# Performance work log

Measured on AMD Instinct MI355X. Metric: run time of the kernel, lower is better.

The kernel has to match this reference:

```python
import jax, jax.numpy as jnp
import numpy as np

B = 64
H = 768  # hidden_dim; x is [B, H, H], split along dim 1 into Q, D of [B, H//2, H]


def setup_inputs() -> dict:
    key = jax.random.key(0)
    kx, kw, kb = jax.random.split(key, 3)
    x = jax.random.normal(kx, (B, H, H), dtype=jnp.float32)
    # nn.Linear(H, H): weight [out, in], bias [out]
    W = jax.random.normal(kw, (H, H), dtype=jnp.float32) * (1.0 / np.sqrt(H))
    b = jax.random.normal(kb, (H,), dtype=jnp.float32) * 0.01
    return {"x": x, "W": W, "b": b}


def reference(x, W, b):
    T = H // 2
    Q = x[:, :T, :]          # [B, T, H]
    D = x[:, T:2 * T, :]     # [B, T, H]
    # Q = tanh(Linear(Q)); torch Linear: y = x @ W^T + b
    Q = jnp.tanh(jnp.einsum('bth,oh->bto', Q, W) + b)  # [B, T, H]
    D_t = jnp.swapaxes(D, 1, 2)                         # [B, H, T]
    L = jnp.einsum('bth,bsh->bts', Q, D)                # [B, T, T]
    A_Q = jnp.swapaxes(jax.nn.softmax(L, axis=1), 1, 2) # softmax over dim 1, then transpose -> [B, T, T]
    C_Q = jnp.matmul(D_t, A_Q)                          # [B, H, T]
    Q_t = jnp.swapaxes(Q, 1, 2)                         # [B, H, T]
    A_D = jax.nn.softmax(L, axis=2)                     # [B, T, T]
    C_D = jnp.matmul(jnp.concatenate((Q_t, C_Q), axis=1), A_D)  # [B, 2H, T]
    C_D_t = jnp.swapaxes(C_D, 1, 2)                     # [B, T, 2H]
    return jnp.concatenate((C_D_t, D), axis=2)          # [B, T, 3H]
```

## Files before the change

kernel.cpp:

```cpp
#include <hip/hip_runtime.h>


typedef __bf16 bf16x8 __attribute__((ext_vector_type(8)));
typedef __bf16 bf16x4 __attribute__((ext_vector_type(4)));
typedef float  f32x4  __attribute__((ext_vector_type(4)));

#define HH 768
#define TT 384

__device__ inline void split8(const float* __restrict__ p, bf16x8& hi, bf16x8& lo) {
    float4 f0 = *(const float4*)p;
    float4 f1 = *(const float4*)(p + 4);
    float f[8] = {f0.x, f0.y, f0.z, f0.w, f1.x, f1.y, f1.z, f1.w};
#pragma unroll
    for (int i = 0; i < 8; i++) {
        __bf16 h = (__bf16)f[i];
        hi[i] = h;
        lo[i] = (__bf16)(f[i] - (float)h);
    }
}

__device__ inline void split8r(float4 f0, float4 f1, bf16x8& hi, bf16x8& lo) {
    float f[8] = {f0.x, f0.y, f0.z, f0.w, f1.x, f1.y, f1.z, f1.w};
#pragma unroll
    for (int i = 0; i < 8; i++) {
        __bf16 h = (__bf16)f[i];
        hi[i] = h;
        lo[i] = (__bf16)(f[i] - (float)h);
    }
}

__device__ inline void gload16(const void* g, void* l) {
    __builtin_amdgcn_global_load_lds(
        (const __attribute__((address_space(1))) unsigned int*)g,
        (__attribute__((address_space(3))) unsigned int*)l, 16, 0, 0);
}

__global__ void splitW_kernel(const float* __restrict__ W, __bf16* __restrict__ Whi,
                              __bf16* __restrict__ Wlo) {
    int idx = blockIdx.x * 256 + threadIdx.x;
    bf16x8 h, l;
    split8(W + (size_t)idx * 8, h, l);
    *(bf16x8*)&Whi[(size_t)idx * 8] = h;
    *(bf16x8*)&Wlo[(size_t)idx * 8] = l;
}

__global__ __launch_bounds__(256) void fused_g1prep_kernel(
    const float* __restrict__ x, const __bf16* __restrict__ Whi,
    const __bf16* __restrict__ Wlo, const float* __restrict__ bias,
    __bf16* __restrict__ Qhi, __bf16* __restrict__ Qlo, __bf16* __restrict__ M4,
    __bf16* __restrict__ Dt, float* __restrict__ out) {
    __shared__ __align__(16) char smem[49152];
    const int tid = threadIdx.x;
    if (blockIdx.x >= 1152) {
        float (*tile)[33] = (float(*)[33])smem;
        int pid = blockIdx.x - 1152;
        int hb = pid % 24, sb = (pid / 24) % 12, b = pid / 288;
        int h0 = hb * 32, s0 = sb * 32;
        int tx = tid & 31, ty = tid >> 5;
        const float* src = x + ((size_t)b * HH + TT) * HH;
        float* outb = out + (size_t)b * TT * 2304;
#pragma unroll
        for (int j = 0; j < 4; j++) {
            int s = s0 + ty + 8 * j, h = h0 + tx;
            float v = src[(size_t)s * HH + h];
            tile[ty + 8 * j][tx] = v;
            outb[(size_t)s * 2304 + 1536 + h] = v;
        }
        __syncthreads();
        __bf16* Dtb = Dt + (size_t)b * HH * TT;
#pragma unroll
        for (int j = 0; j < 4; j++) {
            int h = h0 + ty + 8 * j, s = s0 + tx;
            Dtb[(size_t)h * TT + s] = (__bf16)tile[tx][ty + 8 * j];
        }
        return;
    }
    __bf16* Ah = (__bf16*)smem;
    __bf16* Al = (__bf16*)(smem + 8192);
    __bf16* Bh0 = (__bf16*)(smem + 16384);
    __bf16* Bl0 = (__bf16*)(smem + 32768);
    const int id = blockIdx.x;
    const int nb = id % 6, mb = (id / 6) % 3, b = id / 18;
    const int m_blk = mb * 128, n_blk = nb * 128;
    const int lane = tid & 63, wave = tid >> 6;
    const int wm = wave >> 1, wn = wave & 1;
    const int r15 = lane & 15, quad = lane >> 4;
    const float* Abase = x + (size_t)b * HH * HH;
    const int ra0 = tid >> 2, qa = tid & 3;
    const float* aptr0 = Abase + (size_t)(m_blk + ra0) * HH + qa * 8;
    const float* aptr1 = Abase + (size_t)(m_blk + ra0 + 64) * HH + qa * 8;
    f32x4 acc[4][4];
#pragma unroll
    for (int i = 0; i < 4; i++)
#pragma unroll
        for (int j = 0; j < 4; j++) acc[i][j] = (f32x4){0.f, 0.f, 0.f, 0.f};

    float4 a00 = *(const float4*)(aptr0);
    float4 a01 = *(const float4*)(aptr0 + 4);
    float4 a10 = *(const float4*)(aptr1);
    float4 a11 = *(const float4*)(aptr1 + 4);
#pragma unroll
    for (int it = 0; it < 2; it++) {
        int c = it * 256 + tid, r = c >> 2, q = c & 3;
        gload16(Whi + (size_t)(n_blk + r) * HH + q * 8, Bh0 + c * 8);
        gload16(Wlo + (size_t)(n_blk + r) * HH + q * 8, Bl0 + c * 8);
    }
    int cur = 0;
    for (int k0 = 0; k0 < HH; k0 += 32) {
        {
            bf16x8 h, l;
            split8r(a00, a01, h, l);
            *(bf16x8*)&Ah[tid * 8] = h;
            *(bf16x8*)&Al[tid * 8] = l;
            split8r(a10, a11, h, l);
            *(bf16x8*)&Ah[(256 + tid) * 8] = h;
            *(bf16x8*)&Al[(256 + tid) * 8] = l;
        }
        __syncthreads();
        if (k0 + 32 < HH) {
            a00 = *(const float4*)(aptr0 + k0 + 32);
            a01 = *(const float4*)(aptr0 + k0 + 36);
            a10 = *(const float4*)(aptr1 + k0 + 32);
            a11 = *(const float4*)(aptr1 + k0 + 36);
#pragma unroll
            for (int it = 0; it < 2; it++) {
                int c = it * 256 + tid, r = c >> 2, q = c & 3;
                gload16(Whi + (size_t)(n_blk + r) * HH + k0 + 32 + q * 8,
                        Bh0 + (cur ^ 1) * 4096 + c * 8);
                gload16(Wlo + (size_t)(n_blk + r) * HH + k0 + 32 + q * 8,
                        Bl0 + (cur ^ 1) * 4096 + c * 8);
            }
        }
        bf16x8 ah[4], al[4], bh[4], bl[4];
#pragma unroll
        for (int i = 0; i < 4; i++) {
            int ra = (wm * 64 + i * 16 + r15) * 32 + quad * 8;
            ah[i] = *(const bf16x8*)&Ah[ra];
            al[i] = *(const bf16x8*)&Al[ra];
            int rb = (wn * 64 + i * 16 + r15) * 32 + quad * 8;
            bh[i] = *(const bf16x8*)&Bh0[cur * 4096 + rb];
            bl[i] = *(const bf16x8*)&Bl0[cur * 4096 + rb];
        }
#pragma unroll
        for (int i = 0; i < 4; i++)
#pragma unroll
            for (int j = 0; j < 4; j++) {
                acc[i][j] = __builtin_amdgcn_mfma_f32_16x16x32_bf16(ah[i], bh[j], acc[i][j], 0, 0, 0);
                acc[i][j] = __builtin_amdgcn_mfma_f32_16x16x32_bf16(ah[i], bl[j], acc[i][j], 0, 0, 0);
                acc[i][j] = __builtin_amdgcn_mfma_f32_16x16x32_bf16(al[i], bh[j], acc[i][j], 0, 0, 0);
            }
        __syncthreads();
        cur ^= 1;
    }
    __bf16* Qh = Qhi + (size_t)b * TT * HH;
    __bf16* Ql = Qlo + (size_t)b * TT * HH;
    __bf16* Mb = M4 + (size_t)b * 1536 * TT;
#pragma unroll
    for (int j = 0; j < 4; j++) {
        int col = n_blk + wn * 64 + j * 16 + r15;
        float bv = bias[col];
#pragma unroll
        for (int i = 0; i < 4; i++) {
            int row0 = m_blk + wm * 64 + i * 16 + quad * 4;
            bf16x4 mrow;
#pragma unroll
            for (int r = 0; r < 4; r++) {
                float v = tanhf(acc[i][j][r] + bv);
                __bf16 qh = (__bf16)v;
                Qh[(size_t)(row0 + r) * HH + col] = qh;
                Ql[(size_t)(row0 + r) * HH + col] = (__bf16)(v - (float)qh);
                mrow[r] = qh;
            }
            *(bf16x4*)&Mb[(size_t)col * TT + row0] = mrow;
        }
    }
}

__global__ __launch_bounds__(256) void gemm2_kernel(
    const __bf16* __restrict__ Qhi, const __bf16* __restrict__ Qlo,
    const float* __restrict__ x, float* __restrict__ L) {
    __shared__ __bf16 Ah[2][128 * 32], Al[2][128 * 32];
    __shared__ __bf16 Bh[128 * 32], Bl[128 * 32];
    const int id = blockIdx.x;
    const int xcd = id & 7, kk = id >> 3;
    const int inner = kk % 9, b = (kk / 9) * 8 + xcd;
    const int mb = inner / 3, nb = inner % 3;
    const int m_blk = mb * 128, n_blk = nb * 128;
    const int tid = threadIdx.x, lane = tid & 63, wave = tid >> 6;
    const int wm = wave >> 1, wn = wave & 1;
    const int r15 = lane & 15, quad = lane >> 4;
    const __bf16* Qh = Qhi + (size_t)b * TT * HH;
    const __bf16* Ql = Qlo + (size_t)b * TT * HH;
    const float* Dbase = x + ((size_t)b * HH + TT) * HH;
    const int rb0 = tid >> 2, qb = tid & 3;
    const float* dptr0 = Dbase + (size_t)(n_blk + rb0) * HH + qb * 8;
    const float* dptr1 = Dbase + (size_t)(n_blk + rb0 + 64) * HH + qb * 8;
    f32x4 acc[4][4];
#pragma unroll
    for (int i = 0; i < 4; i++)
#pragma unroll
        for (int j = 0; j < 4; j++) acc[i][j] = (f32x4){0.f, 0.f, 0.f, 0.f};

    float4 d00 = *(const float4*)(dptr0);
    float4 d01 = *(const float4*)(dptr0 + 4);
    float4 d10 = *(const float4*)(dptr1);
    float4 d11 = *(const float4*)(dptr1 + 4);
#pragma unroll
    for (int it = 0; it < 2; it++) {
        int c = it * 256 + tid, r = c >> 2, q = c & 3;
        gload16(Qh + (size_t)(m_blk + r) * HH + q * 8, &Ah[0][c * 8]);
        gload16(Ql + (size_t)(m_blk + r) * HH + q * 8, &Al[0][c * 8]);
    }
    int cur = 0;
    for (int k0 = 0; k0 < HH; k0 += 32) {
        {
            bf16x8 h, l;
            split8r(d00, d01, h, l);
            *(bf16x8*)&Bh[tid * 8] = h;
            *(bf16x8*)&Bl[tid * 8] = l;
            split8r(d10, d11, h, l);
            *(bf16x8*)&Bh[(256 + tid) * 8] = h;
            *(bf16x8*)&Bl[(256 + tid) * 8] = l;
        }
        __syncthreads();
        if (k0 + 32 < HH) {
            d00 = *(const float4*)(dptr0 + k0 + 32);
            d01 = *(const float4*)(dptr0 + k0 + 36);
            d10 = *(const float4*)(dptr1 + k0 + 32);
            d11 = *(const float4*)(dptr1 + k0 + 36);
#pragma unroll
            for (int it = 0; it < 2; it++) {
                int c = it * 256 + tid, r = c >> 2, q = c & 3;
                gload16(Qh + (size_t)(m_blk + r) * HH + k0 + 32 + q * 8, &Ah[cur ^ 1][c * 8]);
                gload16(Ql + (size_t)(m_blk + r) * HH + k0 + 32 + q * 8, &Al[cur ^ 1][c * 8]);
            }
        }
        bf16x8 ah[4], al[4], bh[4], bl[4];
#pragma unroll
        for (int i = 0; i < 4; i++) {
            int ra = (wm * 64 + i * 16 + r15) * 32 + quad * 8;
            ah[i] = *(const bf16x8*)&Ah[cur][ra];
            al[i] = *(const bf16x8*)&Al[cur][ra];
            int rb = (wn * 64 + i * 16 + r15) * 32 + quad * 8;
            bh[i] = *(const bf16x8*)&Bh[rb];
            bl[i] = *(const bf16x8*)&Bl[rb];
        }
#pragma unroll
        for (int i = 0; i < 4; i++)
#pragma unroll
            for (int j = 0; j < 4; j++) {
                acc[i][j] = __builtin_amdgcn_mfma_f32_16x16x32_bf16(ah[i], bh[j], acc[i][j], 0, 0, 0);
                acc[i][j] = __builtin_amdgcn_mfma_f32_16x16x32_bf16(ah[i], bl[j], acc[i][j], 0, 0, 0);
                acc[i][j] = __builtin_amdgcn_mfma_f32_16x16x32_bf16(al[i], bh[j], acc[i][j], 0, 0, 0);
            }
        __syncthreads();
        cur ^= 1;
    }
    float* Lb = L + (size_t)b * TT * TT;
#pragma unroll
    for (int j = 0; j < 4; j++) {
        int col = n_blk + wn * 64 + j * 16 + r15;
#pragma unroll
        for (int i = 0; i < 4; i++) {
            int row0 = m_blk + wm * 64 + i * 16 + quad * 4;
#pragma unroll
            for (int r = 0; r < 4; r++) Lb[(size_t)(row0 + r) * TT + col] = acc[i][j][r];
        }
    }
}

__global__ void sm_fused_kernel(const float* __restrict__ L, __bf16* __restrict__ AQt,
                                __bf16* __restrict__ ADt) {
    __shared__ __align__(16) char smem[49152];
    int b = blockIdx.y;
    int tx = threadIdx.x, ty = threadIdx.y;
    const float* Lb = L + (size_t)b * TT * TT;
    if (blockIdx.x < 6) {
        float (*red)[64] = (float(*)[64])smem;
        int s = blockIdx.x * 64 + tx;
        float mx = -1e30f;
        for (int t = ty; t < TT; t += 4) mx = fmaxf(mx, Lb[(size_t)t * TT + s]);
        red[ty][tx] = mx;
        __syncthreads();
        mx = fmaxf(fmaxf(red[0][tx], red[1][tx]), fmaxf(red[2][tx], red[3][tx]));
        float sum = 0.f;
        for (int t = ty; t < TT; t += 4) sum += __expf(Lb[(size_t)t * TT + s] - mx);
        __syncthreads();
        red[ty][tx] = sum;
        __syncthreads();
        float inv = 1.0f / (red[0][tx] + red[1][tx] + red[2][tx] + red[3][tx]);
        __bf16* Ab = AQt + (size_t)b * TT * TT;
        for (int t = ty; t < TT; t += 4)
            Ab[(size_t)t * TT + s] = (__bf16)(__expf(Lb[(size_t)t * TT + s] - mx) * inv);
    } else {
        __bf16 (*ex)[TT] = (__bf16(*)[TT])smem;
        int t0 = (blockIdx.x - 6) * 64;
        int tid = ty * 64 + tx;
        for (int rr = ty; rr < 64; rr += 4) {
            const float* row = Lb + (size_t)(t0 + rr) * TT;
            float v[6];
            float mx = -1e30f;
#pragma unroll
            for (int k = 0; k < 6; k++) {
                v[k] = row[tx + 64 * k];
                mx = fmaxf(mx, v[k]);
            }
#pragma unroll
            for (int off = 32; off > 0; off >>= 1) mx = fmaxf(mx, __shfl_xor(mx, off));
            float sum = 0.f;
#pragma unroll
            for (int k = 0; k < 6; k++) {
                v[k] = __expf(v[k] - mx);
                sum += v[k];
            }
#pragma unroll
            for (int off = 32; off > 0; off >>= 1) sum += __shfl_xor(sum, off);
            float inv = 1.0f / sum;
#pragma unroll
            for (int k = 0; k < 6; k++) ex[rr][tx + 64 * k] = (__bf16)(v[k] * inv);
        }
        __syncthreads();
        __bf16* Ab = ADt + (size_t)b * TT * TT;
        for (int s = tid; s < TT; s += 256) {
#pragma unroll
            for (int j = 0; j < 8; j++) {
                bf16x8 t8;
#pragma unroll
                for (int e = 0; e < 8; e++) t8[e] = ex[j * 8 + e][s];
                *(bf16x8*)&Ab[(size_t)s * TT + t0 + j * 8] = t8;
            }
        }
    }
}

__global__ __launch_bounds__(256) void gemm3_kernel(
    const __bf16* __restrict__ Dt, const __bf16* __restrict__ AQt,
    __bf16* __restrict__ M4) {
    __shared__ __bf16 As[128 * 32], Bs[128 * 32];
    const int id = blockIdx.x;
    const int xcd = id & 7, kk = id >> 3;
    const int inner = kk % 18, b = (kk / 18) * 8 + xcd;
    const int nb = inner % 3, mb = inner / 3;
    const int m_blk = mb * 128, n_blk = nb * 128;
    const int tid = threadIdx.x, lane = tid & 63, wave = tid >> 6;
    const int wm = wave >> 1, wn = wave & 1;
    const int r15 = lane & 15, quad = lane >> 4;
    const __bf16* Ab = Dt + (size_t)b * HH * TT;
    const __bf16* Bb = AQt + (size_t)b * TT * TT;
    f32x4 acc[4][4];
#pragma unroll
    for (int i = 0; i < 4; i++)
#pragma unroll
        for (int j = 0; j < 4; j++) acc[i][j] = (f32x4){0.f, 0.f, 0.f, 0.f};

    for (int k0 = 0; k0 < TT; k0 += 32) {
#pragma unroll
        for (int it = 0; it < 2; it++) {
            int c = it * 256 + tid;
            int r = c >> 2, q = c & 3;
            gload16(Ab + (size_t)(m_blk + r) * TT + k0 + q * 8, &As[c * 8]);
            gload16(Bb + (size_t)(n_blk + r) * TT + k0 + q * 8, &Bs[c * 8]);
        }
        __syncthreads();
        bf16x8 a[4], bf[4];
#pragma unroll
        for (int i = 0; i < 4; i++) {
            a[i] = *(const bf16x8*)&As[(wm * 64 + i * 16 + r15) * 32 + quad * 8];
            bf[i] = *(const bf16x8*)&Bs[(wn * 64 + i * 16 + r15) * 32 + quad * 8];
        }
#pragma unroll
        for (int i = 0; i < 4; i++)
#pragma unroll
            for (int j = 0; j < 4; j++)
                acc[i][j] = __builtin_amdgcn_mfma_f32_16x16x32_bf16(a[i], bf[j], acc[i][j], 0, 0, 0);
        __syncthreads();
    }
    __bf16* Mb = M4 + (size_t)b * 1536 * TT;
#pragma unroll
    for (int j = 0; j < 4; j++) {
        int col = n_blk + wn * 64 + j * 16 + r15;
#pragma unroll
        for (int i = 0; i < 4; i++) {
            int row0 = m_blk + wm * 64 + i * 16 + quad * 4;
#pragma unroll
            for (int r = 0; r < 4; r++)
                Mb[(size_t)(768 + row0 + r) * TT + col] = (__bf16)acc[i][j][r];
        }
    }
}

__global__ __launch_bounds__(256) void gemm4_kernel(
    const __bf16* __restrict__ ADt, const __bf16* __restrict__ M4,
    float* __restrict__ out) {
    __shared__ __bf16 As[128 * 32], Bs[128 * 32];
    const int id = blockIdx.x;
    const int xcd = id & 7, kk = id >> 3;
    const int inner = kk % 36, b = (kk / 36) * 8 + xcd;
    const int nb = inner % 12, mb = inner / 12;
    const int m_blk = mb * 128, n_blk = nb * 128;
    const int tid = threadIdx.x, lane = tid & 63, wave = tid >> 6;
    const int wm = wave >> 1, wn = wave & 1;
    const int r15 = lane & 15, quad = lane >> 4;
    const __bf16* Ab = ADt + (size_t)b * TT * TT;
    const __bf16* Bb = M4 + (size_t)b * 1536 * TT;
    f32x4 acc[4][4];
#pragma unroll
    for (int i = 0; i < 4; i++)
#pragma unroll
        for (int j = 0; j < 4; j++) acc[i][j] = (f32x4){0.f, 0.f, 0.f, 0.f};

    for (int k0 = 0; k0 < TT; k0 += 32) {
#pragma unroll
        for (int it = 0; it < 2; it++) {
            int c = it * 256 + tid;
            int r = c >> 2, q = c & 3;
            gload16(Ab + (size_t)(m_blk + r) * TT + k0 + q * 8, &As[c * 8]);
            gload16(Bb + (size_t)(n_blk + r) * TT + k0 + q * 8, &Bs[c * 8]);
        }
        __syncthreads();
        bf16x8 a[4], bf[4];
#pragma unroll
        for (int i = 0; i < 4; i++) {
            a[i] = *(const bf16x8*)&As[(wm * 64 + i * 16 + r15) * 32 + quad * 8];
            bf[i] = *(const bf16x8*)&Bs[(wn * 64 + i * 16 + r15) * 32 + quad * 8];
        }
#pragma unroll
        for (int i = 0; i < 4; i++)
#pragma unroll
            for (int j = 0; j < 4; j++)
                acc[i][j] = __builtin_amdgcn_mfma_f32_16x16x32_bf16(a[i], bf[j], acc[i][j], 0, 0, 0);
        __syncthreads();
    }
    float* outb = out + (size_t)b * TT * 2304;
#pragma unroll
    for (int j = 0; j < 4; j++) {
        int col = n_blk + wn * 64 + j * 16 + r15;
#pragma unroll
        for (int i = 0; i < 4; i++) {
            int row0 = m_blk + wm * 64 + i * 16 + quad * 4;
#pragma unroll
            for (int r = 0; r < 4; r++)
                outb[(size_t)(row0 + r) * 2304 + col] = acc[i][j][r];
        }
    }
}

extern "C" void kernel_launch(void* const* d_in, const int* in_sizes, int n_in,
                              void* d_out, int out_size, void* d_ws, size_t ws_size,
                              hipStream_t stream) {
    const float* x = (const float*)d_in[0];
    const float* W = (const float*)d_in[1];
    const float* bias = (const float*)d_in[2];
    float* out = (float*)d_out;
    char* ws = (char*)d_ws;

    __bf16* Qhi = (__bf16*)(ws + 0);
    __bf16* Qlo = (__bf16*)(ws + 37748736);
    __bf16* M4 = (__bf16*)(ws + 75497472);
    __bf16* Dt = (__bf16*)(ws + 150994944);
    float* L = (float*)(ws + 188743680);
    __bf16* AQt = (__bf16*)(ws + 0);
    __bf16* ADt = (__bf16*)(ws + 37748736);
    __bf16* Whi = (__bf16*)(ws + 188743680);
    __bf16* Wlo = Whi + 768 * 768;

    splitW_kernel<<<288, 256, 0, stream>>>(W, Whi, Wlo);
    fused_g1prep_kernel<<<19584, 256, 0, stream>>>(x, Whi, Wlo, bias, Qhi, Qlo, M4, Dt, out);
    gemm2_kernel<<<576, 256, 0, stream>>>(Qhi, Qlo, x, L);
    sm_fused_kernel<<<dim3(12, 64), dim3(64, 4), 0, stream>>>(L, AQt, ADt);
    gemm3_kernel<<<1152, 256, 0, stream>>>(Dt, AQt, M4);
    gemm4_kernel<<<2304, 256, 0, stream>>>(ADt, M4, out);
}
```

Baseline: 716.6 us.

## Halve gemm2 M-tile and co-schedule gemm3 with independent half of gemm4

The gemm2 tile shrinks from 128x128 to 64x128, doubling the block count to improve occupancy and CU coverage. gemm3 and the first half of gemm4 (columns 0-767, which depend only on Q-transposed data already in M4) are merged into one launch so they run concurrently. The second half of gemm4, which consumes gemm3's output, runs in a separate kernel afterwards. This trades reduced launch serialization and tail effects for smaller gemm2 tiles with less data reuse per block.

```diff
diff --git a/kernel.cpp b/kernel.cpp
--- a/kernel.cpp
+++ b/kernel.cpp
@@ -180,13 +180,13 @@
 __global__ __launch_bounds__(256) void gemm2_kernel(
     const __bf16* __restrict__ Qhi, const __bf16* __restrict__ Qlo,
     const float* __restrict__ x, float* __restrict__ L) {
-    __shared__ __bf16 Ah[2][128 * 32], Al[2][128 * 32];
+    __shared__ __bf16 Ah[2][64 * 32], Al[2][64 * 32];
     __shared__ __bf16 Bh[128 * 32], Bl[128 * 32];
     const int id = blockIdx.x;
     const int xcd = id & 7, kk = id >> 3;
-    const int inner = kk % 9, b = (kk / 9) * 8 + xcd;
+    const int inner = kk % 18, b = (kk / 18) * 8 + xcd;
     const int mb = inner / 3, nb = inner % 3;
-    const int m_blk = mb * 128, n_blk = nb * 128;
+    const int m_blk = mb * 64, n_blk = nb * 128;
     const int tid = threadIdx.x, lane = tid & 63, wave = tid >> 6;
     const int wm = wave >> 1, wn = wave & 1;
     const int r15 = lane & 15, quad = lane >> 4;
@@ -196,9 +196,9 @@
     const int rb0 = tid >> 2, qb = tid & 3;
     const float* dptr0 = Dbase + (size_t)(n_blk + rb0) * HH + qb * 8;
     const float* dptr1 = Dbase + (size_t)(n_blk + rb0 + 64) * HH + qb * 8;
-    f32x4 acc[4][4];
-#pragma unroll
-    for (int i = 0; i < 4; i++)
+    f32x4 acc[2][4];
+#pragma unroll
+    for (int i = 0; i < 2; i++)
 #pragma unroll
         for (int j = 0; j < 4; j++) acc[i][j] = (f32x4){0.f, 0.f, 0.f, 0.f};
 
@@ -206,11 +206,10 @@
     float4 d01 = *(const float4*)(dptr0 + 4);
     float4 d10 = *(const float4*)(dptr1);
     float4 d11 = *(const float4*)(dptr1 + 4);
-#pragma unroll
-    for (int it = 0; it < 2; it++) {
-        int c = it * 256 + tid, r = c >> 2, q = c & 3;
-        gload16(Qh + (size_t)(m_blk + r) * HH + q * 8, &Ah[0][c * 8]);
-        gload16(Ql + (size_t)(m_blk + r) * HH + q * 8, &Al[0][c * 8]);
+    {
+        int r = tid >> 2, q = tid & 3;
+        gload16(Qh + (size_t)(m_blk + r) * HH + q * 8, &Ah[0][tid * 8]);
+        gload16(Ql + (size_t)(m_blk + r) * HH + q * 8, &Al[0][tid * 8]);
     }
     int cur = 0;
     for (int k0 = 0; k0 < HH; k0 += 32) {
@@ -229,25 +228,25 @@
             d01 = *(const float4*)(dptr0 + k0 + 36);
             d10 = *(const float4*)(dptr1 + k0 + 32);
             d11 = *(const float4*)(dptr1 + k0 + 36);
-#pragma unroll
-            for (int it = 0; it < 2; it++) {
-                int c = it * 256 + tid, r = c >> 2, q = c & 3;
-                gload16(Qh + (size_t)(m_blk + r) * HH + k0 + 32 + q * 8, &Ah[cur ^ 1][c * 8]);
-                gload16(Ql + (size_t)(m_blk + r) * HH + k0 + 32 + q * 8, &Al[cur ^ 1][c * 8]);
-            }
-        }
-        bf16x8 ah[4], al[4], bh[4], bl[4];
-#pragma unroll
-        for (int i = 0; i < 4; i++) {
-            int ra = (wm * 64 + i * 16 + r15) * 32 + quad * 8;
+            int r = tid >> 2, q = tid & 3;
+            gload16(Qh + (size_t)(m_blk + r) * HH + k0 + 32 + q * 8, &Ah[cur ^ 1][tid * 8]);
+            gload16(Ql + (size_t)(m_blk + r) * HH + k0 + 32 + q * 8, &Al[cur ^ 1][tid * 8]);
+        }
+        bf16x8 ah[2], al[2], bh[4], bl[4];
+#pragma unroll
+        for (int i = 0; i < 2; i++) {
+            int ra = (wm * 32 + i * 16 + r15) * 32 + quad * 8;
             ah[i] = *(const bf16x8*)&Ah[cur][ra];
             al[i] = *(const bf16x8*)&Al[cur][ra];
-            int rb = (wn * 64 + i * 16 + r15) * 32 + quad * 8;
-            bh[i] = *(const bf16x8*)&Bh[rb];
-            bl[i] = *(const bf16x8*)&Bl[rb];
-        }
-#pragma unroll
-        for (int i = 0; i < 4; i++)
+        }
+#pragma unroll
+        for (int j = 0; j < 4; j++) {
+            int rb = (wn * 64 + j * 16 + r15) * 32 + quad * 8;
+            bh[j] = *(const bf16x8*)&Bh[rb];
+            bl[j] = *(const bf16x8*)&Bl[rb];
+        }
+#pragma unroll
+        for (int i = 0; i < 2; i++)
 #pragma unroll
             for (int j = 0; j < 4; j++) {
                 acc[i][j] = __builtin_amdgcn_mfma_f32_16x16x32_bf16(ah[i], bh[j], acc[i][j], 0, 0, 0);
@@ -262,8 +261,8 @@
     for (int j = 0; j < 4; j++) {
         int col = n_blk + wn * 64 + j * 16 + r15;
 #pragma unroll
-        for (int i = 0; i < 4; i++) {
-            int row0 = m_blk + wm * 64 + i * 16 + quad * 4;
+        for (int i = 0; i < 2; i++) {
+            int row0 = m_blk + wm * 32 + i * 16 + quad * 4;
 #pragma unroll
             for (int r = 0; r < 4; r++) Lb[(size_t)(row0 + r) * TT + col] = acc[i][j][r];
         }
@@ -334,70 +333,115 @@
     }
 }
 
-__global__ __launch_bounds__(256) void gemm3_kernel(
+__global__ __launch_bounds__(256) void gemm34_kernel(
     const __bf16* __restrict__ Dt, const __bf16* __restrict__ AQt,
-    __bf16* __restrict__ M4) {
+    const __bf16* __restrict__ ADt, __bf16* __restrict__ M4,
+    float* __restrict__ out) {
     __shared__ __bf16 As[128 * 32], Bs[128 * 32];
-    const int id = blockIdx.x;
-    const int xcd = id & 7, kk = id >> 3;
-    const int inner = kk % 18, b = (kk / 18) * 8 + xcd;
-    const int nb = inner % 3, mb = inner / 3;
-    const int m_blk = mb * 128, n_blk = nb * 128;
     const int tid = threadIdx.x, lane = tid & 63, wave = tid >> 6;
     const int wm = wave >> 1, wn = wave & 1;
     const int r15 = lane & 15, quad = lane >> 4;
-    const __bf16* Ab = Dt + (size_t)b * HH * TT;
-    const __bf16* Bb = AQt + (size_t)b * TT * TT;
     f32x4 acc[4][4];
 #pragma unroll
     for (int i = 0; i < 4; i++)
 #pragma unroll
         for (int j = 0; j < 4; j++) acc[i][j] = (f32x4){0.f, 0.f, 0.f, 0.f};
 
-    for (int k0 = 0; k0 < TT; k0 += 32) {
-#pragma unroll
-        for (int it = 0; it < 2; it++) {
-            int c = it * 256 + tid;
-            int r = c >> 2, q = c & 3;
-            gload16(Ab + (size_t)(m_blk + r) * TT + k0 + q * 8, &As[c * 8]);
-            gload16(Bb + (size_t)(n_blk + r) * TT + k0 + q * 8, &Bs[c * 8]);
-        }
-        __syncthreads();
-        bf16x8 a[4], bf[4];
-#pragma unroll
-        for (int i = 0; i < 4; i++) {
-            a[i] = *(const bf16x8*)&As[(wm * 64 + i * 16 + r15) * 32 + quad * 8];
-            bf[i] = *(const bf16x8*)&Bs[(wn * 64 + i * 16 + r15) * 32 + quad * 8];
-        }
-#pragma unroll
-        for (int i = 0; i < 4; i++)
-#pragma unroll
-            for (int j = 0; j < 4; j++)
-                acc[i][j] = __builtin_amdgcn_mfma_f32_16x16x32_bf16(a[i], bf[j], acc[i][j], 0, 0, 0);
-        __syncthreads();
-    }
-    __bf16* Mb = M4 + (size_t)b * 1536 * TT;
-#pragma unroll
-    for (int j = 0; j < 4; j++) {
-        int col = n_blk + wn * 64 + j * 16 + r15;
-#pragma unroll
-        for (int i = 0; i < 4; i++) {
-            int row0 = m_blk + wm * 64 + i * 16 + quad * 4;
-#pragma unroll
-            for (int r = 0; r < 4; r++)
-                Mb[(size_t)(768 + row0 + r) * TT + col] = (__bf16)acc[i][j][r];
-        }
-    }
-}
-
-__global__ __launch_bounds__(256) void gemm4_kernel(
+    if (blockIdx.x < 1152) {
+        const int id = blockIdx.x;
+        const int xcd = id & 7, kk = id >> 3;
+        const int inner = kk % 18, b = (kk / 18) * 8 + xcd;
+        const int nb = inner % 3, mb = inner / 3;
+        const int m_blk = mb * 128, n_blk = nb * 128;
+        const __bf16* Ab = Dt + (size_t)b * HH * TT;
+        const __bf16* Bb = AQt + (size_t)b * TT * TT;
+        for (int k0 = 0; k0 < TT; k0 += 32) {
+#pragma unroll
+            for (int it = 0; it < 2; it++) {
+                int c = it * 256 + tid;
+                int r = c >> 2, q = c & 3;
+                gload16(Ab + (size_t)(m_blk + r) * TT + k0 + q * 8, &As[c * 8]);
+                gload16(Bb + (size_t)(n_blk + r) * TT + k0 + q * 8, &Bs[c * 8]);
+            }
+            __syncthreads();
+            bf16x8 a[4], bf[4];
+#pragma unroll
+            for (int i = 0; i < 4; i++) {
+                a[i] = *(const bf16x8*)&As[(wm * 64 + i * 16 + r15) * 32 + quad * 8];
+                bf[i] = *(const bf16x8*)&Bs[(wn * 64 + i * 16 + r15) * 32 + quad * 8];
+            }
+#pragma unroll
+            for (int i = 0; i < 4; i++)
+#pragma unroll
+                for (int j = 0; j < 4; j++)
+                    acc[i][j] = __builtin_amdgcn_mfma_f32_16x16x32_bf16(a[i], bf[j], acc[i][j], 0, 0, 0);
+            __syncthreads();
+        }
+        __bf16* Mb = M4 + (size_t)b * 1536 * TT;
+#pragma unroll
+        for (int j = 0; j < 4; j++) {
+            int col = n_blk + wn * 64 + j * 16 + r15;
+#pragma unroll
+            for (int i = 0; i < 4; i++) {
+                int row0 = m_blk + wm * 64 + i * 16 + quad * 4;
+#pragma unroll
+                for (int r = 0; r < 4; r++)
+                    Mb[(size_t)(768 + row0 + r) * TT + col] = (__bf16)acc[i][j][r];
+            }
+        }
+    } else {
+        const int id = blockIdx.x - 1152;
+        const int xcd = id & 7, kk = id >> 3;
+        const int inner = kk % 18, b = (kk / 18) * 8 + xcd;
+        const int nb = inner % 6, mb = inner / 6;
+        const int m_blk = mb * 128, n_blk = nb * 128;
+        const __bf16* Ab = ADt + (size_t)b * TT * TT;
+        const __bf16* Bb = M4 + (size_t)b * 1536 * TT;
+        for (int k0 = 0; k0 < TT; k0 += 32) {
+#pragma unroll
+            for (int it = 0; it < 2; it++) {
+                int c = it * 256 + tid;
+                int r = c >> 2, q = c & 3;
+                gload16(Ab + (size_t)(m_blk + r) * TT + k0 + q * 8, &As[c * 8]);
+                gload16(Bb + (size_t)(n_blk + r) * TT + k0 + q * 8, &Bs[c * 8]);
+            }
+            __syncthreads();
+            bf16x8 a[4], bf[4];
+#pragma unroll
+            for (int i = 0; i < 4; i++) {
+                a[i] = *(const bf16x8*)&As[(wm * 64 + i * 16 + r15) * 32 + quad * 8];
+                bf[i] = *(const bf16x8*)&Bs[(wn * 64 + i * 16 + r15) * 32 + quad * 8];
+            }
+#pragma unroll
+            for (int i = 0; i < 4; i++)
+#pragma unroll
+                for (int j = 0; j < 4; j++)
+                    acc[i][j] = __builtin_amdgcn_mfma_f32_16x16x32_bf16(a[i], bf[j], acc[i][j], 0, 0, 0);
+            __syncthreads();
+        }
+        float* outb = out + (size_t)b * TT * 2304;
+#pragma unroll
+        for (int j = 0; j < 4; j++) {
+            int col = n_blk + wn * 64 + j * 16 + r15;
+#pragma unroll
+            for (int i = 0; i < 4; i++) {
+                int row0 = m_blk + wm * 64 + i * 16 + quad * 4;
+#pragma unroll
+                for (int r = 0; r < 4; r++)
+                    outb[(size_t)(row0 + r) * 2304 + col] = acc[i][j][r];
+            }
+        }
+    }
+}
+
+__global__ __launch_bounds__(256) void gemm4hi_kernel(
     const __bf16* __restrict__ ADt, const __bf16* __restrict__ M4,
     float* __restrict__ out) {
     __shared__ __bf16 As[128 * 32], Bs[128 * 32];
     const int id = blockIdx.x;
     const int xcd = id & 7, kk = id >> 3;
-    const int inner = kk % 36, b = (kk / 36) * 8 + xcd;
-    const int nb = inner % 12, mb = inner / 12;
+    const int inner = kk % 18, b = (kk / 18) * 8 + xcd;
+    const int nb = 6 + inner % 6, mb = inner / 6;
     const int m_blk = mb * 128, n_blk = nb * 128;
     const int tid = threadIdx.x, lane = tid & 63, wave = tid >> 6;
     const int wm = wave >> 1, wn = wave & 1;
@@ -467,8 +511,8 @@
 
     splitW_kernel<<<288, 256, 0, stream>>>(W, Whi, Wlo);
     fused_g1prep_kernel<<<19584, 256, 0, stream>>>(x, Whi, Wlo, bias, Qhi, Qlo, M4, Dt, out);
-    gemm2_kernel<<<576, 256, 0, stream>>>(Qhi, Qlo, x, L);
+    gemm2_kernel<<<1152, 256, 0, stream>>>(Qhi, Qlo, x, L);
     sm_fused_kernel<<<dim3(12, 64), dim3(64, 4), 0, stream>>>(L, AQt, ADt);
-    gemm3_kernel<<<1152, 256, 0, stream>>>(Dt, AQt, M4);
-    gemm4_kernel<<<2304, 256, 0, stream>>>(ADt, M4, out);
-}
+    gemm34_kernel<<<2304, 256, 0, stream>>>(Dt, AQt, ADt, M4, out);
+    gemm4hi_kernel<<<1152, 256, 0, stream>>>(ADt, M4, out);
+}
```

New measurement: 731.0 us. 2.0% more time.

## Split gemm2 K dimension in two and sum partials in softmax kernel

Applied to the files above, without the earlier changes.

The L = Q·D^T GEMM is split along K into two halves, doubling the grid from 576 to 1152 blocks for better CU occupancy. The second partial is written into a currently unused region of the M4 workspace, and the softmax kernel adds the two partials on load. This trades extra fp32 traffic (a second L-sized buffer written and read twice) for more parallelism in the GEMM, and it depends on that M4 region not being overwritten before gemm3 fills it.

```diff
diff --git a/kernel.cpp b/kernel.cpp
--- a/kernel.cpp
+++ b/kernel.cpp
@@ -179,14 +179,16 @@
 
 __global__ __launch_bounds__(256) void gemm2_kernel(
     const __bf16* __restrict__ Qhi, const __bf16* __restrict__ Qlo,
-    const float* __restrict__ x, float* __restrict__ L) {
+    const float* __restrict__ x, float* __restrict__ L, char* __restrict__ M4c) {
     __shared__ __bf16 Ah[2][128 * 32], Al[2][128 * 32];
     __shared__ __bf16 Bh[128 * 32], Bl[128 * 32];
     const int id = blockIdx.x;
     const int xcd = id & 7, kk = id >> 3;
-    const int inner = kk % 9, b = (kk / 9) * 8 + xcd;
-    const int mb = inner / 3, nb = inner % 3;
+    const int inner = kk % 18, b = (kk / 18) * 8 + xcd;
+    const int tile = inner >> 1, ks = inner & 1;
+    const int mb = tile / 3, nb = tile % 3;
     const int m_blk = mb * 128, n_blk = nb * 128;
+    const int kbeg = ks * (HH / 2), kend = kbeg + HH / 2;
     const int tid = threadIdx.x, lane = tid & 63, wave = tid >> 6;
     const int wm = wave >> 1, wn = wave & 1;
     const int r15 = lane & 15, quad = lane >> 4;
@@ -202,18 +204,18 @@
 #pragma unroll
         for (int j = 0; j < 4; j++) acc[i][j] = (f32x4){0.f, 0.f, 0.f, 0.f};
 
-    float4 d00 = *(const float4*)(dptr0);
-    float4 d01 = *(const float4*)(dptr0 + 4);
-    float4 d10 = *(const float4*)(dptr1);
-    float4 d11 = *(const float4*)(dptr1 + 4);
+    float4 d00 = *(const float4*)(dptr0 + kbeg);
+    float4 d01 = *(const float4*)(dptr0 + kbeg + 4);
+    float4 d10 = *(const float4*)(dptr1 + kbeg);
+    float4 d11 = *(const float4*)(dptr1 + kbeg + 4);
 #pragma unroll
     for (int it = 0; it < 2; it++) {
         int c = it * 256 + tid, r = c >> 2, q = c & 3;
-        gload16(Qh + (size_t)(m_blk + r) * HH + q * 8, &Ah[0][c * 8]);
-        gload16(Ql + (size_t)(m_blk + r) * HH + q * 8, &Al[0][c * 8]);
+        gload16(Qh + (size_t)(m_blk + r) * HH + kbeg + q * 8, &Ah[0][c * 8]);
+        gload16(Ql + (size_t)(m_blk + r) * HH + kbeg + q * 8, &Al[0][c * 8]);
     }
     int cur = 0;
-    for (int k0 = 0; k0 < HH; k0 += 32) {
+    for (int k0 = kbeg; k0 < kend; k0 += 32) {
         {
             bf16x8 h, l;
             split8r(d00, d01, h, l);
@@ -224,7 +226,7 @@
             *(bf16x8*)&Bl[(256 + tid) * 8] = l;
         }
         __syncthreads();
-        if (k0 + 32 < HH) {
+        if (k0 + 32 < kend) {
             d00 = *(const float4*)(dptr0 + k0 + 32);
             d01 = *(const float4*)(dptr0 + k0 + 36);
             d10 = *(const float4*)(dptr1 + k0 + 32);
@@ -257,7 +259,8 @@
         __syncthreads();
         cur ^= 1;
     }
-    float* Lb = L + (size_t)b * TT * TT;
+    float* Lb = (ks == 0) ? (L + (size_t)b * TT * TT)
+                          : (float*)(M4c + ((size_t)b * 1536 + 768) * TT * 2);
 #pragma unroll
     for (int j = 0; j < 4; j++) {
         int col = n_blk + wn * 64 + j * 16 + r15;
@@ -270,40 +273,45 @@
     }
 }
 
-__global__ void sm_fused_kernel(const float* __restrict__ L, __bf16* __restrict__ AQt,
-                                __bf16* __restrict__ ADt) {
+__global__ void sm_fused_kernel(const float* __restrict__ L, const char* __restrict__ M4c,
+                                __bf16* __restrict__ AQt, __bf16* __restrict__ ADt) {
     __shared__ __align__(16) char smem[49152];
     int b = blockIdx.y;
     int tx = threadIdx.x, ty = threadIdx.y;
-    const float* Lb = L + (size_t)b * TT * TT;
+    const float* Lb0 = L + (size_t)b * TT * TT;
+    const float* Lb1 = (const float*)(M4c + ((size_t)b * 1536 + 768) * TT * 2);
     if (blockIdx.x < 6) {
         float (*red)[64] = (float(*)[64])smem;
         int s = blockIdx.x * 64 + tx;
         float mx = -1e30f;
-        for (int t = ty; t < TT; t += 4) mx = fmaxf(mx, Lb[(size_t)t * TT + s]);
+        for (int t = ty; t < TT; t += 4)
+            mx = fmaxf(mx, Lb0[(size_t)t * TT + s] + Lb1[(size_t)t * TT + s]);
         red[ty][tx] = mx;
         __syncthreads();
         mx = fmaxf(fmaxf(red[0][tx], red[1][tx]), fmaxf(red[2][tx], red[3][tx]));
         float sum = 0.f;
-        for (int t = ty; t < TT; t += 4) sum += __expf(Lb[(size_t)t * TT + s] - mx);
+        for (int t = ty; t < TT; t += 4)
+            sum += __expf(Lb0[(size_t)t * TT + s] + Lb1[(size_t)t * TT + s] - mx);
         __syncthreads();
         red[ty][tx] = sum;
         __syncthreads();
         float inv = 1.0f / (red[0][tx] + red[1][tx] + red[2][tx] + red[3][tx]);
         __bf16* Ab = AQt + (size_t)b * TT * TT;
         for (int t = ty; t < TT; t += 4)
-            Ab[(size_t)t * TT + s] = (__bf16)(__expf(Lb[(size_t)t * TT + s] - mx) * inv);
+            Ab[(size_t)t * TT + s] =
+                (__bf16)(__expf(Lb0[(size_t)t * TT + s] + Lb1[(size_t)t * TT + s] - mx) * inv);
     } else {
         __bf16 (*ex)[TT] = (__bf16(*)[TT])smem;
         int t0 = (blockIdx.x - 6) * 64;
         int tid = ty * 64 + tx;
         for (int rr = ty; rr < 64; rr += 4) {
-            const float* row = Lb + (size_t)(t0 + rr) * TT;
+            const float* row0 = Lb0 + (size_t)(t0 + rr) * TT;
+            const float* row1 = Lb1 + (size_t)(t0 + rr) * TT;
             float v[6];
             float mx = -1e30f;
 #pragma unroll
             for (int k = 0; k < 6; k++) {
-                v[k] = row[tx + 64 * k];
+                v[k] = row0[tx + 64 * k] + row1[tx + 64 * k];
                 mx = fmaxf(mx, v[k]);
             }
 #pragma unroll
@@ -467,8 +475,8 @@
 
     splitW_kernel<<<288, 256, 0, stream>>>(W, Whi, Wlo);
     fused_g1prep_kernel<<<19584, 256, 0, stream>>>(x, Whi, Wlo, bias, Qhi, Qlo, M4, Dt, out);
-    gemm2_kernel<<<576, 256, 0, stream>>>(Qhi, Qlo, x, L);
-    sm_fused_kernel<<<dim3(12, 64), dim3(64, 4), 0, stream>>>(L, AQt, ADt);
+    gemm2_kernel<<<1152, 256, 0, stream>>>(Qhi, Qlo, x, L, (char*)M4);
+    sm_fused_kernel<<<dim3(12, 64), dim3(64, 4), 0, stream>>>(L, (const char*)M4, AQt, ADt);
     gemm3_kernel<<<1152, 256, 0, stream>>>(Dt, AQt, M4);
     gemm4_kernel<<<2304, 256, 0, stream>>>(ADt, M4, out);
 }
```

After: 728.9 us. No clear change (+1.7%).
